# Kernel tuning notes

Hardware: AMD Instinct MI355X
Metric: run time of the kernel (lower is better)

Reference implementation:

```python
import jax, jax.numpy as jnp
import numpy as np

N_QUERIES = 2000
N_DOCS = 128
FEATURE_DIM = 220
HIDDEN = 768
N_IDS = 65536


def setup_inputs() -> dict:
    key = jax.random.key(0)
    k1, k2, k3, k4, k5 = jax.random.split(key, 5)
    qid = jax.random.randint(k1, (N_IDS,), 0, N_QUERIES)
    did = jax.random.randint(k2, (N_IDS,), 0, N_DOCS)
    input_feature_id = jnp.stack([qid, did], axis=1).astype(jnp.int64)
    feature_table = jax.random.normal(k3, (N_QUERIES, N_DOCS, FEATURE_DIM), dtype=jnp.float32) * 10.0
    W = jax.random.normal(k4, (HIDDEN, FEATURE_DIM), dtype=jnp.float32) * (1.0 / np.sqrt(FEATURE_DIM))
    b = jax.random.normal(k5, (HIDDEN,), dtype=jnp.float32) * 0.01
    return {"input_feature_id": input_feature_id, "feature_table": feature_table, "W": W, "b": b}


def reference(input_feature_id, feature_table, W, b):
    # fused gather over (query, doc) ids: [N, FEATURE_DIM]
    feat = feature_table[input_feature_id[:, 0], input_feature_id[:, 1]]
    # log-sign transform: log(|x| + 1) * sign(x)
    feature_batch = jnp.log(jnp.abs(feat) + 1.0) * jnp.sign(feat)
    # Linear + ReLU (torch Linear: x @ W^T + b)
    output_embeds = jax.nn.relu(feature_batch @ W.T + b)
    return (output_embeds, feature_batch)
```

## Files before the change

### kernel.cpp

```cpp
#include <hip/hip_runtime.h>
#include <hip/hip_bf16.h>

#define M_TOTAL 65536
#define ND      128
#define FDIM    220
#define KPAD    224
#define HID     768
#define G8      28

using bf16_t = __hip_bfloat16;
using bf16x8 = __attribute__((ext_vector_type(8))) short;
using f32x4  = __attribute__((ext_vector_type(4))) float;

struct __align__(16) bf16v8 { bf16_t v[8]; };

__device__ __forceinline__ float slog(float x) {
  return copysignf(log1pf(fabsf(x)), x);
}

__device__ __forceinline__ f32x4 slog4(f32x4 f) {
  f32x4 y;
  y[0] = slog(f[0]); y[1] = slog(f[1]); y[2] = slog(f[2]); y[3] = slog(f[3]);
  return y;
}

__device__ __forceinline__ bf16x8 pack8(f32x4 a, f32x4 b) {
  bf16v8 h;
  h.v[0] = __float2bfloat16(a[0]); h.v[1] = __float2bfloat16(a[1]);
  h.v[2] = __float2bfloat16(a[2]); h.v[3] = __float2bfloat16(a[3]);
  h.v[4] = __float2bfloat16(b[0]); h.v[5] = __float2bfloat16(b[1]);
  h.v[6] = __float2bfloat16(b[2]); h.v[7] = __float2bfloat16(b[3]);
  return __builtin_bit_cast(bf16x8, h);
}

__global__ __launch_bounds__(256) void convert_w_kernel(
    const float* __restrict__ W, bf16_t* __restrict__ Wb)
{
  const int j   = blockIdx.x * 256 + threadIdx.x;
  const int row = j / G8;
  const int g   = j % G8;

  const float* src = W + (size_t)row * FDIM + g * 8;
  const f32x4 f0 = *(const f32x4*)src;
  f32x4 f1;
  if (g < 27) f1 = *(const f32x4*)(src + 4);
  else        { f1[0] = 0.f; f1[1] = 0.f; f1[2] = 0.f; f1[3] = 0.f; }
  *(bf16v8*)(Wb + (size_t)row * KPAD + g * 8) = __builtin_bit_cast(bf16v8, pack8(f0, f1));
}

__global__ __launch_bounds__(256, 2) void fused_gather_gemm_kernel(
    const int2* __restrict__ ids, const float* __restrict__ table,
    const bf16_t* __restrict__ Wb, const float* __restrict__ bias,
    float* __restrict__ out, float* __restrict__ fb)
{
  const int tid  = threadIdx.x;
  const int bm   = blockIdx.x;
  const int wave = tid >> 6;
  const int lane = tid & 63;
  const int l15  = lane & 15;
  const int q    = lane >> 4;

  const int rbase = bm * 128 + wave * 32;

  bf16x8 af[7][2];
#pragma unroll
  for (int mi = 0; mi < 2; ++mi) {
    const int grow = rbase + mi * 16 + l15;
    const int2 p   = ids[grow];
    const float* srow = table + ((size_t)p.x * ND + p.y) * FDIM;
    float*       frow = fb + (size_t)grow * FDIM;
#pragma unroll
    for (int kb = 0; kb < 7; ++kb) {
      const int  c0   = kb * 32 + q * 8;
      const bool tail = (kb == 6) && (q == 3);
      f32x4 lo = *(const f32x4*)(srow + c0);
      f32x4 hi;
      if (!tail) hi = *(const f32x4*)(srow + c0 + 4);
      else       { hi[0] = 0.f; hi[1] = 0.f; hi[2] = 0.f; hi[3] = 0.f; }
      lo = slog4(lo);
      hi = slog4(hi);
      __builtin_nontemporal_store(lo, (f32x4*)(frow + c0));
      if (!tail)
        __builtin_nontemporal_store(hi, (f32x4*)(frow + c0 + 4));
      af[kb][mi] = pack8(lo, hi);
    }
  }

  for (int bn = 0; bn < 6; ++bn) {
    f32x4 acc[2][8];
#pragma unroll
    for (int i = 0; i < 2; ++i)
#pragma unroll
      for (int j = 0; j < 8; ++j) acc[i][j] = (f32x4){0.f, 0.f, 0.f, 0.f};

    const bf16_t* Wbase = Wb + (size_t)(bn * 128 + l15) * KPAD + q * 8;

#pragma unroll
    for (int kb = 0; kb < 7; ++kb) {
      bf16x8 bg[8];
#pragma unroll
      for (int ni = 0; ni < 8; ++ni)
        bg[ni] = *(const bf16x8*)(Wbase + (size_t)ni * 16 * KPAD + kb * 32);
#pragma unroll
      for (int mi = 0; mi < 2; ++mi)
#pragma unroll
        for (int ni = 0; ni < 8; ++ni)
          acc[mi][ni] = __builtin_amdgcn_mfma_f32_16x16x32_bf16(
              af[kb][mi], bg[ni], acc[mi][ni], 0, 0, 0);
    }

    const int col0 = bn * 128 + l15;
    const int row0 = rbase + q * 4;

    float bv[8];
#pragma unroll
    for (int ni = 0; ni < 8; ++ni) bv[ni] = bias[col0 + ni * 16];

#pragma unroll
    for (int mi = 0; mi < 2; ++mi) {
#pragma unroll
      for (int r = 0; r < 4; ++r) {
        const size_t rowoff = (size_t)(row0 + mi * 16 + r) * HID;
#pragma unroll
        for (int ni = 0; ni < 8; ++ni) {
          float v = acc[mi][ni][r] + bv[ni];
          v = v > 0.f ? v : 0.f;
          __builtin_nontemporal_store(v, out + rowoff + col0 + ni * 16);
        }
      }
    }
  }
}

extern "C" void kernel_launch(void* const* d_in, const int* in_sizes, int n_in,
                              void* d_out, int out_size, void* d_ws, size_t ws_size,
                              hipStream_t stream) {
  (void)in_sizes; (void)n_in; (void)out_size; (void)ws_size;

  const int2*  ids   = (const int2*)d_in[0];
  const float* table = (const float*)d_in[1];
  const float* W     = (const float*)d_in[2];
  const float* bias  = (const float*)d_in[3];

  float* out_embeds = (float*)d_out;
  float* fb_f32     = (float*)d_out + (size_t)M_TOTAL * HID;

  bf16_t* Wb = (bf16_t*)d_ws;

  convert_w_kernel<<<(HID * G8) / 256, 256, 0, stream>>>(W, Wb);

  fused_gather_gemm_kernel<<<M_TOTAL / 128, 256, 0, stream>>>(
      ids, table, Wb, bias, out_embeds, fb_f32);
}
```

Measured before the change: 458.6 us.

## Halve rows per wave to raise occupancy and drop nontemporal stores

```diff
diff --git a/kernel.cpp b/kernel.cpp
--- a/kernel.cpp
+++ b/kernel.cpp
@@ -48,7 +48,7 @@
   *(bf16v8*)(Wb + (size_t)row * KPAD + g * 8) = __builtin_bit_cast(bf16v8, pack8(f0, f1));
 }
 
-__global__ __launch_bounds__(256, 2) void fused_gather_gemm_kernel(
+__global__ __launch_bounds__(256, 4) void fused_gather_gemm_kernel(
     const int2* __restrict__ ids, const float* __restrict__ table,
     const bf16_t* __restrict__ Wb, const float* __restrict__ bias,
     float* __restrict__ out, float* __restrict__ fb)
@@ -60,38 +60,33 @@
   const int l15  = lane & 15;
   const int q    = lane >> 4;
 
-  const int rbase = bm * 128 + wave * 32;
+  const int rbase = bm * 64 + wave * 16;
+  const int grow  = rbase + l15;
 
-  bf16x8 af[7][2];
+  const int2 p = ids[grow];
+  const float* srow = table + ((size_t)p.x * ND + p.y) * FDIM;
+  float*       frow = fb + (size_t)grow * FDIM;
+
+  bf16x8 af[7];
 #pragma unroll
-  for (int mi = 0; mi < 2; ++mi) {
-    const int grow = rbase + mi * 16 + l15;
-    const int2 p   = ids[grow];
-    const float* srow = table + ((size_t)p.x * ND + p.y) * FDIM;
-    float*       frow = fb + (size_t)grow * FDIM;
-#pragma unroll
-    for (int kb = 0; kb < 7; ++kb) {
-      const int  c0   = kb * 32 + q * 8;
-      const bool tail = (kb == 6) && (q == 3);
-      f32x4 lo = *(const f32x4*)(srow + c0);
-      f32x4 hi;
-      if (!tail) hi = *(const f32x4*)(srow + c0 + 4);
-      else       { hi[0] = 0.f; hi[1] = 0.f; hi[2] = 0.f; hi[3] = 0.f; }
-      lo = slog4(lo);
-      hi = slog4(hi);
-      __builtin_nontemporal_store(lo, (f32x4*)(frow + c0));
-      if (!tail)
-        __builtin_nontemporal_store(hi, (f32x4*)(frow + c0 + 4));
-      af[kb][mi] = pack8(lo, hi);
-    }
+  for (int kb = 0; kb < 7; ++kb) {
+    const int  c0   = kb * 32 + q * 8;
+    const bool tail = (kb == 6) && (q == 3);
+    f32x4 lo = *(const f32x4*)(srow + c0);
+    f32x4 hi;
+    if (!tail) hi = *(const f32x4*)(srow + c0 + 4);
+    else       { hi[0] = 0.f; hi[1] = 0.f; hi[2] = 0.f; hi[3] = 0.f; }
+    lo = slog4(lo);
+    if (!tail) hi = slog4(hi);
+    *(f32x4*)(frow + c0) = lo;
+    if (!tail) *(f32x4*)(frow + c0 + 4) = hi;
+    af[kb] = pack8(lo, hi);
   }
 
   for (int bn = 0; bn < 6; ++bn) {
-    f32x4 acc[2][8];
+    f32x4 acc[8];
 #pragma unroll
-    for (int i = 0; i < 2; ++i)
-#pragma unroll
-      for (int j = 0; j < 8; ++j) acc[i][j] = (f32x4){0.f, 0.f, 0.f, 0.f};
+    for (int j = 0; j < 8; ++j) acc[j] = (f32x4){0.f, 0.f, 0.f, 0.f};
 
     const bf16_t* Wbase = Wb + (size_t)(bn * 128 + l15) * KPAD + q * 8;
 
@@ -102,11 +97,9 @@
       for (int ni = 0; ni < 8; ++ni)
         bg[ni] = *(const bf16x8*)(Wbase + (size_t)ni * 16 * KPAD + kb * 32);
 #pragma unroll
-      for (int mi = 0; mi < 2; ++mi)
-#pragma unroll
-        for (int ni = 0; ni < 8; ++ni)
-          acc[mi][ni] = __builtin_amdgcn_mfma_f32_16x16x32_bf16(
-              af[kb][mi], bg[ni], acc[mi][ni], 0, 0, 0);
+      for (int ni = 0; ni < 8; ++ni)
+        acc[ni] = __builtin_amdgcn_mfma_f32_16x16x32_bf16(
+            af[kb], bg[ni], acc[ni], 0, 0, 0);
     }
 
     const int col0 = bn * 128 + l15;
@@ -117,16 +110,12 @@
     for (int ni = 0; ni < 8; ++ni) bv[ni] = bias[col0 + ni * 16];
 
 #pragma unroll
-    for (int mi = 0; mi < 2; ++mi) {
+    for (int r = 0; r < 4; ++r) {
+      const size_t rowoff = (size_t)(row0 + r) * HID;
 #pragma unroll
-      for (int r = 0; r < 4; ++r) {
-        const size_t rowoff = (size_t)(row0 + mi * 16 + r) * HID;
-#pragma unroll
-        for (int ni = 0; ni < 8; ++ni) {
-          float v = acc[mi][ni][r] + bv[ni];
-          v = v > 0.f ? v : 0.f;
-          __builtin_nontemporal_store(v, out + rowoff + col0 + ni * 16);
-        }
+      for (int ni = 0; ni < 8; ++ni) {
+        float v = acc[ni][r] + bv[ni];
+        out[rowoff + col0 + ni * 16] = v > 0.f ? v : 0.f;
       }
     }
   }
@@ -149,6 +138,6 @@
 
   convert_w_kernel<<<(HID * G8) / 256, 256, 0, stream>>>(W, Wb);
 
-  fused_gather_gemm_kernel<<<M_TOTAL / 128, 256, 0, stream>>>(
+  fused_gather_gemm_kernel<<<M_TOTAL / 64, 256, 0, stream>>>(
       ids, table, Wb, bias, out_embeds, fb_f32);
 }
```

New measurement: 464.4 us. No clear change (+1.3%).
